# Performance work log

Hardware: AMD Instinct MI355X
Metric: run time of the kernel (lower is better)

The kernel has to match this reference:

```python
import jax, jax.numpy as jnp
import numpy as np

B, T, C = 2, 4096, 768
H = 12
D = C // H  # head_dim = 64

def setup_inputs() -> dict:
    key = jax.random.key(0)
    ks = jax.random.split(key, 5)
    s = 1.0 / np.sqrt(C)
    return {
        "x": jax.random.normal(ks[0], (B, T, C), dtype=jnp.float32),
        "qkv_w": jax.random.normal(ks[1], (C, 3 * C), dtype=jnp.float32) * s,
        "qkv_b": jax.random.normal(ks[2], (3 * C,), dtype=jnp.float32) * 0.02,
        "out_w": jax.random.normal(ks[3], (C, C), dtype=jnp.float32) * s,
        "out_b": jax.random.normal(ks[4], (C,), dtype=jnp.float32) * 0.02,
    }

def reference(x, qkv_w, qkv_b, out_w, out_b):
    b, t, c = x.shape
    qkv = x @ qkv_w + qkv_b                      # [B,T,3C]
    q, k, v = jnp.split(qkv, 3, axis=-1)
    # [B,T,C] -> [B,H,T,D]
    q = q.reshape(b, t, H, D).transpose(0, 2, 1, 3)
    k = k.reshape(b, t, H, D).transpose(0, 2, 1, 3)
    v = v.reshape(b, t, H, D).transpose(0, 2, 1, 3)
    scale = 1.0 / np.sqrt(D)
    attn = jnp.einsum('bhqd,bhkd->bhqk', q, k) * scale  # [B,H,T,T]
    causal = jnp.tril(jnp.ones((t, t), dtype=bool))
    attn = jnp.where(causal, attn, -jnp.inf)
    attn = jax.nn.softmax(attn, axis=-1)
    y = jnp.einsum('bhqk,bhkd->bhqd', attn, v)           # [B,H,T,D]
    y = y.transpose(0, 2, 1, 3).reshape(b, t, c)
    return y @ out_w + out_b
```

## Files before the change

### kernel.cpp

```cpp
#include <hip/hip_runtime.h>
#include <hip/hip_bf16.h>

#define T_SEQ 4096
#define C_DIM 768
#define H_NUM 12
#define D_HEAD 64
#define N3    2304
#define BHN   24

typedef __bf16 bf16x8 __attribute__((ext_vector_type(8)));
typedef float  f32x4  __attribute__((ext_vector_type(4)));

__device__ inline unsigned short f2b(float f) {
    unsigned int x = __float_as_uint(f);
    unsigned int r = (x + 0x7FFFu + ((x >> 16) & 1u)) >> 16;
    return (unsigned short)r;
}

__device__ inline unsigned int pack_trunc(float lo, float hi) {
    return __builtin_amdgcn_perm(__float_as_uint(hi), __float_as_uint(lo), 0x07060302u);
}

__device__ inline void load_lds16(const unsigned short* g, unsigned short* l) {
    __builtin_amdgcn_global_load_lds(
        (const __attribute__((address_space(1))) unsigned int*)(g),
        (__attribute__((address_space(3))) unsigned int*)(l),
        16, 0, 0);
}

__device__ inline void transpose_tile(const float* __restrict__ in,
                                      unsigned short* __restrict__ out,
                                      unsigned short* Ts, int k0, int n0,
                                      int R, int Cc, int tid)
{
    #pragma unroll
    for (int it = 0; it < 4; ++it) {
        int idx = tid + it * 256;
        int r = idx >> 4, c4 = idx & 15;
        float4 v = *reinterpret_cast<const float4*>(&in[(size_t)(k0 + r) * Cc + n0 + c4 * 4]);
        Ts[(c4 * 4 + 0) * 72 + r] = f2b(v.x);
        Ts[(c4 * 4 + 1) * 72 + r] = f2b(v.y);
        Ts[(c4 * 4 + 2) * 72 + r] = f2b(v.z);
        Ts[(c4 * 4 + 3) * 72 + r] = f2b(v.w);
    }
    __syncthreads();
    #pragma unroll
    for (int it = 0; it < 2; ++it) {
        int idx = tid + it * 256;
        int row = idx >> 3, ch = idx & 7;
        *reinterpret_cast<uint4*>(&out[(size_t)(n0 + row) * R + k0 + ch * 8]) =
            *reinterpret_cast<const uint4*>(&Ts[row * 72 + ch * 8]);
    }
}

__global__ __launch_bounds__(256) void prep(
    const float* __restrict__ x, const float* __restrict__ qkv_w,
    const float* __restrict__ out_w,
    unsigned short* __restrict__ xb, unsigned short* __restrict__ wtq,
    unsigned short* __restrict__ wto)
{
    __shared__ unsigned short Ts[64 * 72];
    const int b = blockIdx.x, tid = threadIdx.x;
    if (b < 6144) {
        int idx = b * 256 + tid;
        float4 v = reinterpret_cast<const float4*>(x)[idx];
        ushort4 u;
        u.x = f2b(v.x); u.y = f2b(v.y); u.z = f2b(v.z); u.w = f2b(v.w);
        reinterpret_cast<ushort4*>(xb)[idx] = u;
    } else if (b < 6576) {
        int bb = b - 6144;
        transpose_tile(qkv_w, wtq, Ts, (bb % 12) * 64, (bb / 12) * 64, C_DIM, N3, tid);
    } else {
        int bb = b - 6576;
        transpose_tile(out_w, wto, Ts, (bb % 12) * 64, (bb / 12) * 64, C_DIM, C_DIM, tid);
    }
}

__global__ __launch_bounds__(256) void qkv_gemm(
    const unsigned short* __restrict__ xb, const unsigned short* __restrict__ wt,
    const float* __restrict__ bias,
    unsigned short* __restrict__ Q, unsigned short* __restrict__ K,
    unsigned short* __restrict__ Vt)
{
    __shared__ unsigned short SH[128 * 128];
    unsigned short* As = SH;
    unsigned short* Bs = SH + 128 * 64;
    const int tid  = threadIdx.x;
    const int m0   = blockIdx.x * 128;
    const int n0   = blockIdx.y * 128;
    const int lane = tid & 63;
    const int wv   = tid >> 6;
    const int wr   = wv >> 1, wc = wv & 1;
    const int quad = lane >> 4;
    const int lr   = lane & 15;
    const int srow = lane >> 3;
    const int dch  = (lane & 7) ^ srow;

    f32x4 acc[4][4] = {};

    for (int kk = 0; kk < C_DIM; kk += 64) {
        __syncthreads();
        #pragma unroll
        for (int i = 0; i < 4; ++i) {
            int inst = wv * 4 + i;
            int r = inst * 8 + srow;
            load_lds16(xb + (size_t)(m0 + r) * C_DIM + kk + dch * 8, As + inst * 512);
            load_lds16(wt + (size_t)(n0 + r) * C_DIM + kk + dch * 8, Bs + inst * 512);
        }
        __syncthreads();
        #pragma unroll
        for (int k2 = 0; k2 < 2; ++k2) {
            bf16x8 af[4], bf[4];
            #pragma unroll
            for (int mt = 0; mt < 4; ++mt)
                af[mt] = *reinterpret_cast<const bf16x8*>(
                    &As[(wr * 64 + mt * 16 + lr) * 64 + (((k2 * 4 + quad) ^ (lr & 7)) * 8)]);
            #pragma unroll
            for (int nt = 0; nt < 4; ++nt)
                bf[nt] = *reinterpret_cast<const bf16x8*>(
                    &Bs[(wc * 64 + nt * 16 + lr) * 64 + (((k2 * 4 + quad) ^ (lr & 7)) * 8)]);
            #pragma unroll
            for (int mt = 0; mt < 4; ++mt)
                #pragma unroll
                for (int nt = 0; nt < 4; ++nt)
                    acc[mt][nt] = __builtin_amdgcn_mfma_f32_16x16x32_bf16(af[mt], bf[nt], acc[mt][nt], 0, 0, 0);
        }
    }

    const int whichblk = n0 / C_DIM;
    if (whichblk == 2) {
        __syncthreads();
        #pragma unroll
        for (int nt = 0; nt < 4; ++nt) {
            int dp = wc * 64 + nt * 16 + lr;
            float bj = bias[n0 + dp];
            #pragma unroll
            for (int mt = 0; mt < 4; ++mt) {
                int t0 = wr * 64 + mt * 16 + quad * 4;
                ushort4 u;
                u.x = f2b(acc[mt][nt][0] + bj);
                u.y = f2b(acc[mt][nt][1] + bj);
                u.z = f2b(acc[mt][nt][2] + bj);
                u.w = f2b(acc[mt][nt][3] + bj);
                int cs = (t0 >> 2) ^ ((dp & 15) << 1);
                *reinterpret_cast<ushort4*>(&SH[dp * 128 + cs * 4]) = u;
            }
        }
        __syncthreads();
        const int bb = m0 >> 12;
        const int t_base = m0 & 4095;
        const int h_base = (n0 - 2 * C_DIM) >> 6;
        #pragma unroll
        for (int i = 0; i < 8; ++i) {
            int idx = i * 256 + tid;
            int row = idx >> 4, cc = idx & 15;
            int pc = ((2 * cc) ^ ((row & 15) << 1)) * 4;
            uint4 val = *reinterpret_cast<const uint4*>(&SH[row * 128 + pc]);
            int head = h_base + (row >> 6);
            int d = row & 63;
            *reinterpret_cast<uint4*>(
                &Vt[((size_t)(bb * H_NUM + head) * D_HEAD + d) * T_SEQ + t_base + cc * 8]) = val;
        }
    } else {
        const int head0 = ((n0 % C_DIM) + wc * 64) >> 6;
        #pragma unroll
        for (int nt = 0; nt < 4; ++nt) {
            int d = nt * 16 + lr;
            float bj = bias[n0 + wc * 64 + nt * 16 + lr];
            #pragma unroll
            for (int mt = 0; mt < 4; ++mt) {
                #pragma unroll
                for (int reg = 0; reg < 4; ++reg) {
                    int i = m0 + wr * 64 + mt * 16 + quad * 4 + reg;
                    int bb = i >> 12, t = i & 4095;
                    float val = acc[mt][nt][reg] + bj;
                    size_t base = (size_t)(bb * H_NUM + head0) * T_SEQ + t;
                    if (whichblk == 0)
                        Q[base * D_HEAD + d] = f2b(val * 0.18033688011f);
                    else
                        K[base * D_HEAD + d] = f2b(val);
                }
            }
        }
    }
}

__global__ __launch_bounds__(256, 3) void flash_attn(
    const unsigned short* __restrict__ Q, const unsigned short* __restrict__ K,
    const unsigned short* __restrict__ Vt, unsigned short* __restrict__ Y)
{
    __shared__ unsigned short Ks[2][64 * 64];
    __shared__ unsigned short Vs[2][64 * 64];
    __shared__ unsigned short Ps[2][64 * 72];
    const int tid  = threadIdx.x;
    const int lane = tid & 63;
    const int wv   = tid >> 6;
    const int quad = lane >> 4;
    const int lr   = lane & 15;
    const int srow = lane >> 3;
    const int dch  = (lane & 7) ^ srow;

    const int bid = blockIdx.x;
    const int qt  = 31 - (bid / BHN);
    const int bh  = bid % BHN;
    const int q0  = qt * 128;
    const int diag0 = 2 * qt;
    const int last  = diag0 + 1;

    const unsigned short* Qb = Q  + (size_t)bh * T_SEQ * D_HEAD;
    const unsigned short* Kb = K  + (size_t)bh * T_SEQ * D_HEAD;
    const unsigned short* Vb = Vt + (size_t)bh * D_HEAD * T_SEQ;

    bf16x8 bQ[2][2];
    #pragma unroll
    for (int h = 0; h < 2; ++h)
        #pragma unroll
        for (int k2 = 0; k2 < 2; ++k2)
            bQ[h][k2] = *reinterpret_cast<const bf16x8*>(
                &Qb[(size_t)(q0 + h * 64 + wv * 16 + lr) * D_HEAD + k2 * 32 + quad * 8]);

    bf16x8 ones;
    #pragma unroll
    for (int i = 0; i < 8; ++i) ones[i] = (__bf16)1.0f;
    const f32x4 zf = {};

    f32x4 oacc[2][4] = {};
    f32x4 lacc[2] = {};

    unsigned short* Pw0 = &Ps[0][(wv * 16) * 72];
    unsigned short* Pw1 = &Ps[1][(wv * 16) * 72];

    #pragma unroll
    for (int i = 0; i < 2; ++i) {
        int inst = wv * 2 + i;
        int r = inst * 8 + srow;
        load_lds16(Kb + (size_t)r * D_HEAD + dch * 8, Ks[0] + inst * 512);
        load_lds16(Vb + (size_t)r * T_SEQ + dch * 8, Vs[0] + inst * 512);
    }

    for (int kt = 0; kt <= last; ++kt) {
        const int buf = kt & 1;
        __syncthreads();

        if (kt < last) {
            #pragma unroll
            for (int i = 0; i < 2; ++i) {
                int inst = wv * 2 + i;
                int r = inst * 8 + srow;
                load_lds16(Kb + (size_t)((kt + 1) * 64 + r) * D_HEAD + dch * 8,
                           Ks[buf ^ 1] + inst * 512);
                load_lds16(Vb + (size_t)r * T_SEQ + (kt + 1) * 64 + dch * 8,
                           Vs[buf ^ 1] + inst * 512);
            }
        }

        const bool doh0 = (kt <= diag0);

        bf16x8 aK[4][2];
        #pragma unroll
        for (int mt = 0; mt < 4; ++mt)
            #pragma unroll
            for (int k2 = 0; k2 < 2; ++k2)
                aK[mt][k2] = *reinterpret_cast<const bf16x8*>(
                    &Ks[buf][(mt * 16 + lr) * 64 + (((k2 * 4 + quad) ^ (lr & 7)) * 8)]);

        f32x4 st0[4], st1[4];
        #pragma unroll
        for (int mt = 0; mt < 4; ++mt) {
            st1[mt] = __builtin_amdgcn_mfma_f32_16x16x32_bf16(aK[mt][0], bQ[1][0], zf, 0, 0, 0);
            st1[mt] = __builtin_amdgcn_mfma_f32_16x16x32_bf16(aK[mt][1], bQ[1][1], st1[mt], 0, 0, 0);
        }
        if (doh0) {
            #pragma unroll
            for (int mt = 0; mt < 4; ++mt) {
                st0[mt] = __builtin_amdgcn_mfma_f32_16x16x32_bf16(aK[mt][0], bQ[0][0], zf, 0, 0, 0);
                st0[mt] = __builtin_amdgcn_mfma_f32_16x16x32_bf16(aK[mt][1], bQ[0][1], st0[mt], 0, 0, 0);
            }
        }

        if (kt == diag0) {
            int qg = q0 + wv * 16 + lr;
            #pragma unroll
            for (int mt = 0; mt < 4; ++mt)
                #pragma unroll
                for (int reg = 0; reg < 4; ++reg)
                    if (kt * 64 + mt * 16 + quad * 4 + reg > qg) st0[mt][reg] = -INFINITY;
        }
        if (kt == last) {
            int qg = q0 + 64 + wv * 16 + lr;
            #pragma unroll
            for (int mt = 0; mt < 4; ++mt)
                #pragma unroll
                for (int reg = 0; reg < 4; ++reg)
                    if (kt * 64 + mt * 16 + quad * 4 + reg > qg) st1[mt][reg] = -INFINITY;
        }

        #pragma unroll
        for (int mt = 0; mt < 4; ++mt) {
            #pragma unroll
            for (int reg = 0; reg < 4; ++reg)
                st1[mt][reg] = __builtin_amdgcn_exp2f(st1[mt][reg]);
            uint2 u;
            u.x = pack_trunc(st1[mt][0], st1[mt][1]);
            u.y = pack_trunc(st1[mt][2], st1[mt][3]);
            *reinterpret_cast<uint2*>(&Pw1[lr * 72 + mt * 16 + quad * 4]) = u;
        }
        if (doh0) {
            #pragma unroll
            for (int mt = 0; mt < 4; ++mt) {
                #pragma unroll
                for (int reg = 0; reg < 4; ++reg)
                    st0[mt][reg] = __builtin_amdgcn_exp2f(st0[mt][reg]);
                uint2 u;
                u.x = pack_trunc(st0[mt][0], st0[mt][1]);
                u.y = pack_trunc(st0[mt][2], st0[mt][3]);
                *reinterpret_cast<uint2*>(&Pw0[lr * 72 + mt * 16 + quad * 4]) = u;
            }
        }

        bf16x8 aV[4][2];
        #pragma unroll
        for (int mt = 0; mt < 4; ++mt)
            #pragma unroll
            for (int k2 = 0; k2 < 2; ++k2)
                aV[mt][k2] = *reinterpret_cast<const bf16x8*>(
                    &Vs[buf][(mt * 16 + lr) * 64 + (((k2 * 4 + quad) ^ (lr & 7)) * 8)]);

        if (doh0) {
            bf16x8 bP0 = *reinterpret_cast<const bf16x8*>(&Pw0[lr * 72 + quad * 8]);
            bf16x8 bP1 = *reinterpret_cast<const bf16x8*>(&Pw0[lr * 72 + 32 + quad * 8]);
            #pragma unroll
            for (int dt = 0; dt < 4; ++dt) {
                oacc[0][dt] = __builtin_amdgcn_mfma_f32_16x16x32_bf16(aV[dt][0], bP0, oacc[0][dt], 0, 0, 0);
                oacc[0][dt] = __builtin_amdgcn_mfma_f32_16x16x32_bf16(aV[dt][1], bP1, oacc[0][dt], 0, 0, 0);
            }
            lacc[0] = __builtin_amdgcn_mfma_f32_16x16x32_bf16(ones, bP0, lacc[0], 0, 0, 0);
            lacc[0] = __builtin_amdgcn_mfma_f32_16x16x32_bf16(ones, bP1, lacc[0], 0, 0, 0);
        }
        {
            bf16x8 bP0 = *reinterpret_cast<const bf16x8*>(&Pw1[lr * 72 + quad * 8]);
            bf16x8 bP1 = *reinterpret_cast<const bf16x8*>(&Pw1[lr * 72 + 32 + quad * 8]);
            #pragma unroll
            for (int dt = 0; dt < 4; ++dt) {
                oacc[1][dt] = __builtin_amdgcn_mfma_f32_16x16x32_bf16(aV[dt][0], bP0, oacc[1][dt], 0, 0, 0);
                oacc[1][dt] = __builtin_amdgcn_mfma_f32_16x16x32_bf16(aV[dt][1], bP1, oacc[1][dt], 0, 0, 0);
            }
            lacc[1] = __builtin_amdgcn_mfma_f32_16x16x32_bf16(ones, bP0, lacc[1], 0, 0, 0);
            lacc[1] = __builtin_amdgcn_mfma_f32_16x16x32_bf16(ones, bP1, lacc[1], 0, 0, 0);
        }
    }

    const int bb = bh / H_NUM, hh = bh % H_NUM;
    #pragma unroll
    for (int h = 0; h < 2; ++h) {
        float inv = 1.f / lacc[h][0];
        int q = q0 + h * 64 + wv * 16 + lr;
        #pragma unroll
        for (int dt = 0; dt < 4; ++dt) {
            ushort4 u;
            u.x = f2b(oacc[h][dt][0] * inv);
            u.y = f2b(oacc[h][dt][1] * inv);
            u.z = f2b(oacc[h][dt][2] * inv);
            u.w = f2b(oacc[h][dt][3] * inv);
            *reinterpret_cast<ushort4*>(
                &Y[(size_t)(bb * T_SEQ + q) * C_DIM + hh * 64 + dt * 16 + quad * 4]) = u;
        }
    }
}

__global__ __launch_bounds__(256) void out_gemm(
    const unsigned short* __restrict__ Y, const unsigned short* __restrict__ wt,
    const float* __restrict__ bias, float* __restrict__ out)
{
    __shared__ unsigned short As[128 * 64];
    __shared__ unsigned short Bs[64 * 64];
    const int tid  = threadIdx.x;
    const int m0   = blockIdx.x * 128;
    const int n0   = blockIdx.y * 64;
    const int lane = tid & 63;
    const int wv   = tid >> 6;
    const int wr   = wv >> 1, wc = wv & 1;
    const int quad = lane >> 4;
    const int lr   = lane & 15;
    const int srow = lane >> 3;
    const int dch  = (lane & 7) ^ srow;

    f32x4 acc[4][2] = {};

    for (int kk = 0; kk < C_DIM; kk += 64) {
        __syncthreads();
        #pragma unroll
        for (int i = 0; i < 4; ++i) {
            int inst = wv * 4 + i;
            int r = inst * 8 + srow;
            load_lds16(Y + (size_t)(m0 + r) * C_DIM + kk + dch * 8, As + inst * 512);
        }
        #pragma unroll
        for (int i = 0; i < 2; ++i) {
            int inst = wv * 2 + i;
            int r = inst * 8 + srow;
            load_lds16(wt + (size_t)(n0 + r) * C_DIM + kk + dch * 8, Bs + inst * 512);
        }
        __syncthreads();
        #pragma unroll
        for (int k2 = 0; k2 < 2; ++k2) {
            bf16x8 af[4], bf[2];
            #pragma unroll
            for (int mt = 0; mt < 4; ++mt)
                af[mt] = *reinterpret_cast<const bf16x8*>(
                    &As[(wr * 64 + mt * 16 + lr) * 64 + (((k2 * 4 + quad) ^ (lr & 7)) * 8)]);
            #pragma unroll
            for (int nt = 0; nt < 2; ++nt)
                bf[nt] = *reinterpret_cast<const bf16x8*>(
                    &Bs[(wc * 32 + nt * 16 + lr) * 64 + (((k2 * 4 + quad) ^ (lr & 7)) * 8)]);
            #pragma unroll
            for (int mt = 0; mt < 4; ++mt)
                #pragma unroll
                for (int nt = 0; nt < 2; ++nt)
                    acc[mt][nt] = __builtin_amdgcn_mfma_f32_16x16x32_bf16(af[mt], bf[nt], acc[mt][nt], 0, 0, 0);
        }
    }

    #pragma unroll
    for (int nt = 0; nt < 2; ++nt) {
        int j = n0 + wc * 32 + nt * 16 + lr;
        float bj = bias[j];
        #pragma unroll
        for (int mt = 0; mt < 4; ++mt)
            #pragma unroll
            for (int reg = 0; reg < 4; ++reg) {
                int i = m0 + wr * 64 + mt * 16 + quad * 4 + reg;
                out[(size_t)i * C_DIM + j] = acc[mt][nt][reg] + bj;
            }
    }
}

extern "C" void kernel_launch(void* const* d_in, const int* in_sizes, int n_in,
                              void* d_out, int out_size, void* d_ws, size_t ws_size,
                              hipStream_t stream) {
    const float* x     = (const float*)d_in[0];
    const float* qkv_w = (const float*)d_in[1];
    const float* qkv_b = (const float*)d_in[2];
    const float* out_w = (const float*)d_in[3];
    const float* out_b = (const float*)d_in[4];
    float* out = (float*)d_out;

    unsigned short* xb  = (unsigned short*)d_ws;
    unsigned short* wtq = xb  + (size_t)8192 * 768;
    unsigned short* wto = wtq + (size_t)2304 * 768;
    unsigned short* Qs  = wto + (size_t)768 * 768;
    unsigned short* Kg  = Qs  + (size_t)BHN * T_SEQ * D_HEAD;
    unsigned short* Vt  = Kg  + (size_t)BHN * T_SEQ * D_HEAD;
    unsigned short* Y   = xb;

    prep      <<<6720, 256, 0, stream>>>(x, qkv_w, out_w, xb, wtq, wto);
    qkv_gemm  <<<dim3(64, 18), 256, 0, stream>>>(xb, wtq, qkv_b, Qs, Kg, Vt);
    flash_attn<<<dim3(32 * BHN), 256, 0, stream>>>(Qs, Kg, Vt, Y);
    out_gemm  <<<dim3(64, 12), 256, 0, stream>>>(Y, wto, out_b, out);
}
```

Measured before the change: 230.1 us.

## Load K/V tiles directly from global memory and remap blocks per XCD

Removes the double-buffered LDS staging of K and V tiles along with the per-iteration block barrier. Each wave now reads its K and V MFMA operands straight from global memory. Block indices are remapped so that the heads assigned to one XCD stay together, which should improve L2 reuse of K/V. Dropping the LDS copy saves shared memory and synchronisation. The cost is that every wave fetches the same K/V data redundantly from global/L2 with no software prefetch, so the MFMAs may stall on memory latency.

```diff
diff --git a/kernel.cpp b/kernel.cpp
--- a/kernel.cpp
+++ b/kernel.cpp
@@ -189,20 +189,18 @@
     const unsigned short* __restrict__ Q, const unsigned short* __restrict__ K,
     const unsigned short* __restrict__ Vt, unsigned short* __restrict__ Y)
 {
-    __shared__ unsigned short Ks[2][64 * 64];
-    __shared__ unsigned short Vs[2][64 * 64];
     __shared__ unsigned short Ps[2][64 * 72];
     const int tid  = threadIdx.x;
     const int lane = tid & 63;
     const int wv   = tid >> 6;
     const int quad = lane >> 4;
     const int lr   = lane & 15;
-    const int srow = lane >> 3;
-    const int dch  = (lane & 7) ^ srow;
 
     const int bid = blockIdx.x;
-    const int qt  = 31 - (bid / BHN);
-    const int bh  = bid % BHN;
+    const int xcd = bid & 7;
+    const int jj  = (bid >> 3) % 3;
+    const int bh  = xcd * 3 + jj;
+    const int qt  = 31 - (bid / 24);
     const int q0  = qt * 128;
     const int diag0 = 2 * qt;
     const int last  = diag0 + 1;
@@ -230,31 +228,9 @@
     unsigned short* Pw0 = &Ps[0][(wv * 16) * 72];
     unsigned short* Pw1 = &Ps[1][(wv * 16) * 72];
 
-    #pragma unroll
-    for (int i = 0; i < 2; ++i) {
-        int inst = wv * 2 + i;
-        int r = inst * 8 + srow;
-        load_lds16(Kb + (size_t)r * D_HEAD + dch * 8, Ks[0] + inst * 512);
-        load_lds16(Vb + (size_t)r * T_SEQ + dch * 8, Vs[0] + inst * 512);
-    }
-
     for (int kt = 0; kt <= last; ++kt) {
-        const int buf = kt & 1;
-        __syncthreads();
-
-        if (kt < last) {
-            #pragma unroll
-            for (int i = 0; i < 2; ++i) {
-                int inst = wv * 2 + i;
-                int r = inst * 8 + srow;
-                load_lds16(Kb + (size_t)((kt + 1) * 64 + r) * D_HEAD + dch * 8,
-                           Ks[buf ^ 1] + inst * 512);
-                load_lds16(Vb + (size_t)r * T_SEQ + (kt + 1) * 64 + dch * 8,
-                           Vs[buf ^ 1] + inst * 512);
-            }
-        }
-
         const bool doh0 = (kt <= diag0);
+        const unsigned short* Kt = Kb + (size_t)kt * 64 * D_HEAD;
 
         bf16x8 aK[4][2];
         #pragma unroll
@@ -262,7 +238,7 @@
             #pragma unroll
             for (int k2 = 0; k2 < 2; ++k2)
                 aK[mt][k2] = *reinterpret_cast<const bf16x8*>(
-                    &Ks[buf][(mt * 16 + lr) * 64 + (((k2 * 4 + quad) ^ (lr & 7)) * 8)]);
+                    &Kt[(mt * 16 + lr) * D_HEAD + k2 * 32 + quad * 8]);
 
         f32x4 st0[4], st1[4];
         #pragma unroll
@@ -324,7 +300,7 @@
             #pragma unroll
             for (int k2 = 0; k2 < 2; ++k2)
                 aV[mt][k2] = *reinterpret_cast<const bf16x8*>(
-                    &Vs[buf][(mt * 16 + lr) * 64 + (((k2 * 4 + quad) ^ (lr & 7)) * 8)]);
+                    &Vb[(size_t)(mt * 16 + lr) * T_SEQ + kt * 64 + k2 * 32 + quad * 8]);
 
         if (doh0) {
             bf16x8 bP0 = *reinterpret_cast<const bf16x8*>(&Pw0[lr * 72 + quad * 8]);
```

After: 382.3 us. 1.66x slower.
